# Performance work log

Hardware: AMD Instinct MI355X
Metric: run time of the kernel (lower is better)

The kernel has to match this reference:

```python
import jax, jax.numpy as jnp
import numpy as np
import math

N_HEAD = 16
ROPE_BASE = 10000.0


def _rope(xh):
    # xh: [B, H, T, D]; rotate full head dim using half-split (GPT-NeoX style)
    B, H, T, D = xh.shape
    theta = 1.0 / (ROPE_BASE ** (jnp.arange(0, D, 2, dtype=jnp.float32) / D))  # [D/2]
    idx_theta = jnp.arange(T, dtype=jnp.float32)[:, None] * theta[None, :]      # [T, D/2]
    idx_theta2 = jnp.concatenate([idx_theta, idx_theta], axis=1)                 # [T, D]
    cos = jnp.cos(idx_theta2)[None, None]                                        # [1,1,T,D]
    sin = jnp.sin(idx_theta2)[None, None]
    d2 = D // 2
    neg_half = jnp.concatenate([-xh[..., d2:], xh[..., :d2]], axis=-1)
    return xh * cos + neg_half * sin


def setup_inputs() -> dict:
    key = jax.random.key(0)
    k1, k2, k3 = jax.random.split(key, 3)
    B, T, C = 2, 2048, 2048
    x = jax.random.normal(k1, (B, T, C), dtype=jnp.float32)
    w_attn = jax.random.normal(k2, (C, 3 * C), dtype=jnp.float32) * (1.0 / math.sqrt(C))
    w_proj = jax.random.normal(k3, (C, C), dtype=jnp.float32) * (1.0 / math.sqrt(C))
    return {"x": x, "w_attn": w_attn, "w_proj": w_proj}


def reference(x, w_attn, w_proj):
    B, T, C = x.shape
    H = N_HEAD
    D = C // H
    qkv = x @ w_attn                                   # [B,T,3C]
    q, k, v = jnp.split(qkv, 3, axis=-1)
    # [B,T,C] -> [B,H,T,D]
    to_heads = lambda t: t.reshape(B, T, H, D).transpose(0, 2, 1, 3)
    q, k, v = to_heads(q), to_heads(k), to_heads(v)
    q = _rope(q)
    k = _rope(k)
    att = jnp.einsum('bhqd,bhkd->bhqk', q, k) * (1.0 / math.sqrt(D))
    causal = jnp.tril(jnp.ones((T, T), dtype=bool))
    att = jnp.where(causal[None, None], att, -jnp.inf)
    att = jax.nn.softmax(att, axis=-1)
    y = jnp.einsum('bhqk,bhkd->bhqd', att, v)          # [B,H,T,D]
    y = y.transpose(0, 2, 1, 3).reshape(B, T, C)
    return y @ w_proj
```

## Files before the change

kernel.cpp:

```cpp
#include <hip/hip_runtime.h>
#include <hip/hip_bf16.h>
#include <math.h>

typedef __bf16 bf16;
typedef __bf16 bf16x8 __attribute__((ext_vector_type(8)));
typedef float f32x4 __attribute__((ext_vector_type(4)));
typedef float f32x16 __attribute__((ext_vector_type(16)));
typedef unsigned int u32x2 __attribute__((ext_vector_type(2)));
typedef unsigned int u32x4 __attribute__((ext_vector_type(4)));

#define MFMA16(a, b, c) __builtin_amdgcn_mfma_f32_16x16x32_bf16((a), (b), (c), 0, 0, 0)
#define MFMA32(a, b, c) __builtin_amdgcn_mfma_f32_32x32x16_bf16((a), (b), (c), 0, 0, 0)

static constexpr int Bsz = 2, Tsz = 2048, Csz = 2048, Hn = 16, Dh = 128;
static constexpr float ATTN_SCALE = 0.08838834764831845f;

__device__ __forceinline__ void gld16(const void* src, void* dst) {
    __builtin_amdgcn_global_load_lds((__attribute__((address_space(1))) void*)src,
                                     (__attribute__((address_space(3))) void*)dst,
                                     16, 0, 0);
}

__device__ __forceinline__ unsigned cvt_pk_bf16(float lo, float hi) {
    unsigned r;
    asm("v_cvt_pk_bf16_f32 %0, %1, %2" : "=v"(r) : "v"(lo), "v"(hi));
    return r;
}

__device__ __forceinline__ bf16x8 make_pfrag(float p0, float p1, float p2, float p3,
                                             float p4, float p5, float p6, float p7) {
    unsigned a0 = cvt_pk_bf16(p0, p1), a1 = cvt_pk_bf16(p2, p3);
    unsigned b0 = cvt_pk_bf16(p4, p5), b1 = cvt_pk_bf16(p6, p7);
    asm volatile("v_permlane32_swap_b32 %0, %1" : "+v"(a0), "+v"(b0));
    asm volatile("v_permlane32_swap_b32 %0, %1" : "+v"(a1), "+v"(b1));
    u32x4 w = {a0, a1, b0, b1};
    return __builtin_bit_cast(bf16x8, w);
}

__global__ __launch_bounds__(256) void cast_x_kernel(const float* __restrict__ x,
                                                     bf16* __restrict__ o, int n8) {
    int i = blockIdx.x * 256 + threadIdx.x;
    if (i >= n8) return;
    const float4* x4 = (const float4*)x;
    float4 a = x4[2 * i], b = x4[2 * i + 1];
    bf16x8 v;
    v[0] = (bf16)a.x; v[1] = (bf16)a.y; v[2] = (bf16)a.z; v[3] = (bf16)a.w;
    v[4] = (bf16)b.x; v[5] = (bf16)b.y; v[6] = (bf16)b.z; v[7] = (bf16)b.w;
    ((bf16x8*)o)[i] = v;
}

template <typename TIN>
__global__ __launch_bounds__(256) void transpose_cast_kernel(const TIN* __restrict__ in,
                                                             bf16* __restrict__ out,
                                                             int R, int Cc) {
    __shared__ float tile[64][65];
    const int tx = threadIdx.x, ty = threadIdx.y;
    in  += (size_t)blockIdx.z * R * Cc;
    out += (size_t)blockIdx.z * R * Cc;
    const int c0 = blockIdx.x * 64, r0 = blockIdx.y * 64;
#pragma unroll
    for (int j = 0; j < 16; ++j) {
        int rr = ty + j * 4;
        tile[rr][tx] = (float)in[(size_t)(r0 + rr) * Cc + c0 + tx];
    }
    __syncthreads();
#pragma unroll
    for (int j = 0; j < 16; ++j) {
        int cc = ty + j * 4;
        out[(size_t)(c0 + cc) * R + r0 + tx] = (bf16)tile[tx][cc];
    }
}

__global__ __launch_bounds__(256) void cossin_kernel(float2* __restrict__ cs) {
    int idx = blockIdx.x * 256 + threadIdx.x;
    int t = idx >> 6, i = idx & 63;
    float theta = 1.0f / powf(10000.0f, (float)(2 * i) / 128.0f);
    float ang = (float)t * theta;
    cs[idx] = make_float2(cosf(ang), sinf(ang));
}

__global__ __launch_bounds__(512, 2)
void gemm384_qkv(const bf16* __restrict__ A, const bf16* __restrict__ Bt,
                 bf16* __restrict__ Oq, bf16* __restrict__ Ok, bf16* __restrict__ Ov,
                 const float2* __restrict__ cs, int K) {
    __shared__ bf16 sA[2][128 * 64];
    __shared__ bf16 sB[2][384 * 64];
    const int tid = threadIdx.x, lane = tid & 63, wid = tid >> 6;
    const int wm = wid >> 2, wn = wid & 3;
    const int lo16 = lane & 15, hi4 = lane >> 4;

    const int cpx = gridDim.x >> 3;
    const int swz = (blockIdx.x & 7) * cpx + (blockIdx.x >> 3);
    const int by = swz & 31;
    const int bx = swz >> 5;
    const int row0 = by << 7, col0 = bx * 384;

    const int srow = tid >> 3;
    const int swzoff = (((tid & 7) ^ ((tid >> 3) & 7)) << 3);
    const bf16* srcA = A  + (size_t)(row0 + srow) * K + swzoff;
    const bf16* srcB = Bt + (size_t)(col0 + srow) * K + swzoff;
    const size_t K64 = (size_t)K * 64;
    char* const ldsA = (char*)&sA[0][0];
    char* const ldsB = (char*)&sB[0][0];
    const int wuo = wid << 10;

    auto issueA = [&](int c, int kt) {
        const bf16* s = srcA + (size_t)kt * 64;
        gld16(s,       ldsA + c * 16384 + 0    + wuo);
        gld16(s + K64, ldsA + c * 16384 + 8192 + wuo);
    };
    auto issueB3lo = [&](int c, int kt) {
        const bf16* s = srcB + (size_t)kt * 64;
        gld16(s,           ldsB + c * 49152 + 0     + wuo);
        gld16(s + K64,     ldsB + c * 49152 + 8192  + wuo);
        gld16(s + 2 * K64, ldsB + c * 49152 + 16384 + wuo);
    };
    auto issueB3hi = [&](int c, int kt) {
        const bf16* s = srcB + (size_t)kt * 64 + 3 * K64;
        gld16(s,           ldsB + c * 49152 + 24576 + wuo);
        gld16(s + K64,     ldsB + c * 49152 + 32768 + wuo);
        gld16(s + 2 * K64, ldsB + c * 49152 + 40960 + wuo);
    };
    auto ldF = [&](const char* buf, int row, int ks) {
        return *(const bf16x8*)(buf + row * 128 + ((((ks << 2) + hi4) ^ (row & 7)) << 4));
    };

    const int arow = (wm << 6) + lo16;
    const int brow = (wn << 4) + lo16;

    f32x4 acc[4][6] = {};
    const int nkt = K >> 6;

    issueB3lo(0, 0); issueB3hi(0, 0); issueA(0, 0);
    if (nkt > 1) {
        issueA(1, 1);
        asm volatile("s_waitcnt vmcnt(2)" ::: "memory");
    } else {
        asm volatile("s_waitcnt vmcnt(0)" ::: "memory");
    }
    __builtin_amdgcn_s_barrier();

    for (int kt = 0; kt < nkt; ++kt) {
        const int c = kt & 1;
        const char* bufA = ldsA + c * 16384;
        const char* bufB = ldsB + c * 49152;
        bf16x8 af[4][2], bq[2][2];
#pragma unroll
        for (int i = 0; i < 4; ++i) {
            af[i][0] = ldF(bufA, arow + (i << 4), 0);
            af[i][1] = ldF(bufA, arow + (i << 4), 1);
        }
#pragma unroll
        for (int j = 0; j < 2; ++j) {
            bq[j][0] = ldF(bufB, brow + (j << 6), 0);
            bq[j][1] = ldF(bufB, brow + (j << 6), 1);
        }
        if (kt + 1 < nkt) issueB3lo(c ^ 1, kt + 1);
        __builtin_amdgcn_s_barrier();
        asm volatile("s_waitcnt lgkmcnt(0)" ::: "memory");
        __builtin_amdgcn_sched_barrier(0);
        __builtin_amdgcn_s_setprio(1);
#pragma unroll
        for (int ks = 0; ks < 2; ++ks)
#pragma unroll
            for (int i = 0; i < 4; ++i)
#pragma unroll
                for (int j = 0; j < 2; ++j)
                    acc[i][j] = MFMA16(af[i][ks], bq[j][ks], acc[i][j]);
        __builtin_amdgcn_s_setprio(0);
        __builtin_amdgcn_s_barrier();
#pragma unroll
        for (int j = 0; j < 2; ++j) {
            bq[j][0] = ldF(bufB, brow + ((j + 2) << 6), 0);
            bq[j][1] = ldF(bufB, brow + ((j + 2) << 6), 1);
        }
        if (kt + 1 < nkt) issueB3hi(c ^ 1, kt + 1);
        __builtin_amdgcn_s_barrier();
        asm volatile("s_waitcnt lgkmcnt(0)" ::: "memory");
        __builtin_amdgcn_sched_barrier(0);
        __builtin_amdgcn_s_setprio(1);
#pragma unroll
        for (int ks = 0; ks < 2; ++ks)
#pragma unroll
            for (int i = 0; i < 4; ++i)
#pragma unroll
                for (int j = 0; j < 2; ++j)
                    acc[i][j + 2] = MFMA16(af[i][ks], bq[j][ks], acc[i][j + 2]);
        __builtin_amdgcn_s_setprio(0);
        __builtin_amdgcn_s_barrier();
#pragma unroll
        for (int j = 0; j < 2; ++j) {
            bq[j][0] = ldF(bufB, brow + ((j + 4) << 6), 0);
            bq[j][1] = ldF(bufB, brow + ((j + 4) << 6), 1);
        }
        if (kt + 2 < nkt) issueA(c, kt + 2);
        __builtin_amdgcn_s_barrier();
        asm volatile("s_waitcnt lgkmcnt(0)" ::: "memory");
        __builtin_amdgcn_sched_barrier(0);
        __builtin_amdgcn_s_setprio(1);
#pragma unroll
        for (int ks = 0; ks < 2; ++ks)
#pragma unroll
            for (int i = 0; i < 4; ++i)
#pragma unroll
                for (int j = 0; j < 2; ++j)
                    acc[i][j + 4] = MFMA16(af[i][ks], bq[j][ks], acc[i][j + 4]);
        __builtin_amdgcn_s_setprio(0);
        if (kt + 2 < nkt)      asm volatile("s_waitcnt vmcnt(2)" ::: "memory");
        else if (kt + 1 < nkt) asm volatile("s_waitcnt vmcnt(0)" ::: "memory");
        __builtin_amdgcn_s_barrier();
    }

    const int d = (wn << 4) + lo16;
#pragma unroll
    for (int p = 0; p < 3; ++p) {
        const int gcb = col0 + (p << 7);
        const int seg = gcb >> 11;
        const int hb = (gcb >> 7) & 15;
        if (seg < 2) {
            bf16* dst0 = (seg == 0) ? Oq : Ok;
            const float qs = (seg == 0) ? ATTN_SCALE : 1.0f;
#pragma unroll
            for (int mi = 0; mi < 4; ++mi)
#pragma unroll
                for (int r = 0; r < 4; ++r) {
                    const int gm = row0 + (wm << 6) + (mi << 4) + (hi4 << 2) + r;
                    const int b = gm >> 11, t = gm & 2047;
                    const float2 csv = cs[t * 64 + d];
                    bf16* drow = dst0 + ((((size_t)b * Hn + hb) * Tsz + t) << 7);
                    const float vlo = acc[mi][2 * p][r];
                    const float vhi = acc[mi][2 * p + 1][r];
                    drow[d]      = (bf16)((vlo * csv.x - vhi * csv.y) * qs);
                    drow[d + 64] = (bf16)((vhi * csv.x + vlo * csv.y) * qs);
                }
        } else {
#pragma unroll
            for (int mi = 0; mi < 4; ++mi)
#pragma unroll
                for (int r = 0; r < 4; ++r) {
                    const int gm = row0 + (wm << 6) + (mi << 4) + (hi4 << 2) + r;
                    const int b = gm >> 11, t = gm & 2047;
                    bf16* drow = Ov + ((((size_t)b * Hn + hb) * Tsz + t) << 7);
                    drow[d]      = (bf16)acc[mi][2 * p][r];
                    drow[d + 64] = (bf16)acc[mi][2 * p + 1][r];
                }
        }
    }
}

__global__ __launch_bounds__(256)
void gemm128_bt(const bf16* __restrict__ A, const bf16* __restrict__ Bt,
                float* __restrict__ Cf, int M, int N, int K) {
    __shared__ bf16 sA[128 * 64];
    __shared__ bf16 sB[128 * 64];
    const int tid = threadIdx.x;
    const int lane = tid & 63, wv = tid >> 6;
    const int wr = wv >> 1, wc = wv & 1;
    const int lo16 = lane & 15, hi4 = lane >> 4;
    const int row0 = blockIdx.y << 7, col0 = blockIdx.x << 7;

    f32x4 acc[4][4] = {};

    const int nkt = K >> 6;
    for (int kt = 0; kt < nkt; ++kt) {
        const int kbase = kt << 6;
#pragma unroll
        for (int c = 0; c < 4; ++c) {
            const int o16 = (c << 8) + tid;
            const int row = o16 >> 3, u = o16 & 7;
            const int colel = kbase + ((u ^ (row & 7)) << 3);
            gld16(A  + (size_t)(row0 + row) * K + colel,
                  (char*)sA + (((c << 8) + (wv << 6)) << 4));
            gld16(Bt + (size_t)(col0 + row) * K + colel,
                  (char*)sB + (((c << 8) + (wv << 6)) << 4));
        }
        __syncthreads();
#pragma unroll
        for (int ks = 0; ks < 2; ++ks) {
            bf16x8 af[4], bfv[4];
#pragma unroll
            for (int mi = 0; mi < 4; ++mi) {
                const int ar = (wr << 6) + (mi << 4) + lo16;
                af[mi] = *(const bf16x8*)((const char*)sA + ar * 128 +
                          (((ks << 6) + (hi4 << 4)) ^ ((ar & 7) << 4)));
            }
#pragma unroll
            for (int ni = 0; ni < 4; ++ni) {
                const int bc = (wc << 4) + (ni << 5) + lo16;
                bfv[ni] = *(const bf16x8*)((const char*)sB + bc * 128 +
                           (((ks << 6) + (hi4 << 4)) ^ ((bc & 7) << 4)));
            }
#pragma unroll
            for (int mi = 0; mi < 4; ++mi)
#pragma unroll
                for (int ni = 0; ni < 4; ++ni)
                    acc[mi][ni] = MFMA16(af[mi], bfv[ni], acc[mi][ni]);
        }
        __syncthreads();
    }

#pragma unroll
    for (int mi = 0; mi < 4; ++mi)
#pragma unroll
        for (int r = 0; r < 4; ++r) {
            const int gm = row0 + (wr << 6) + (mi << 4) + (hi4 << 2) + r;
            float* crow = Cf + (size_t)gm * N + col0 + (wc << 4) + lo16;
#pragma unroll
            for (int ni = 0; ni < 4; ++ni)
                crow[ni << 5] = acc[mi][ni][r];
        }
}

__device__ __forceinline__ void stage_tile(const bf16* __restrict__ Kb,
                                           const bf16* __restrict__ Vtb,
                                           bf16* sKc, bf16* sVc, int k0, int tid) {
#pragma unroll
    for (int c = 0; c < 4; ++c) {
        const int off = (c << 12) + (tid << 4);
        const int row = off >> 8, u = (off >> 4) & 15;
        gld16(Kb + (size_t)(k0 + row) * Dh + ((u ^ (row & 7)) << 3), (char*)sKc + off);
        const int dv = off >> 7, uv = (off >> 4) & 7;
        gld16(Vtb + (size_t)dv * Tsz + k0 + ((uv ^ (dv & 7)) << 3), (char*)sVc + off);
    }
}

__global__ __launch_bounds__(256, 2)
void attn_kernel(const bf16* __restrict__ Q, const bf16* __restrict__ K,
                 const bf16* __restrict__ Vt, bf16* __restrict__ Y) {
    __shared__ bf16 sK[2][64 * 128];
    __shared__ bf16 sV[2][128 * 64];
    const int tid = threadIdx.x, lane = tid & 63, wv = tid >> 6;
    const int lo32 = lane & 31, hl = lane >> 5;

    const int i = blockIdx.x;
    const int g = i >> 5;
    const int bh = i & 31;
    const int t = (i < 256) ? (15 - g) : (g - 8);
    const int b = bh >> 4, h = bh & 15;

    const int q0 = t << 7;
    const int q0w = q0 + (wv << 5);
    const int qg = q0w + lo32;

    const bf16* Kb  = K  + (size_t)bh * (Tsz * Dh);
    const bf16* Vtb = Vt + (size_t)bh * (Tsz * Dh);
    const bf16* Qp  = Q  + (size_t)bh * (Tsz * Dh) + (size_t)qg * Dh;

    bf16x8 qf[8];
#pragma unroll
    for (int kc = 0; kc < 8; ++kc)
        qf[kc] = *(const bf16x8*)(Qp + (kc << 4) + (hl << 3));

    float m = -1e30f, lsum = 0.f;
    f32x16 o[4] = {};

    const int nt_block = 2 * t + 2;
    const int nt_warp = ((q0w + 31) >> 6) + 1;

    stage_tile(Kb, Vtb, &sK[0][0], &sV[0][0], 0, tid);

    int cur = 0;
    for (int kt = 0; kt < nt_block; ++kt) {
        __syncthreads();
        if (kt + 1 < nt_block)
            stage_tile(Kb, Vtb, &sK[cur ^ 1][0], &sV[cur ^ 1][0], (kt + 1) << 6, tid);
        if (kt < nt_warp) {
            const int k0 = kt << 6;
            const bf16* kbuf = &sK[cur][0];
            const bf16* vbuf = &sV[cur][0];
            f32x16 s0 = {}, s1 = {};
            const int swk = lo32 & 7;
            __builtin_amdgcn_s_setprio(1);
#pragma unroll
            for (int kc = 0; kc < 8; ++kc) {
                bf16x8 kf0 = *(const bf16x8*)((const char*)kbuf + lo32 * 256 +
                              ((((kc << 1) + hl) ^ swk) << 4));
                s0 = MFMA32(kf0, qf[kc], s0);
                bf16x8 kf1 = *(const bf16x8*)((const char*)kbuf + (32 + lo32) * 256 +
                              ((((kc << 1) + hl) ^ swk) << 4));
                s1 = MFMA32(kf1, qf[kc], s1);
            }
            __builtin_amdgcn_s_setprio(0);

            const bool bnd = (k0 + 63 > q0w);
            if (bnd) {
#pragma unroll
                for (int r = 0; r < 16; ++r) {
                    const int kl = (r & 3) + ((r >> 2) << 3) + (hl << 2);
                    if (k0 + kl > qg)      s0[r] = -1e30f;
                    if (k0 + 32 + kl > qg) s1[r] = -1e30f;
                }
            }
            float pm = s0[0];
#pragma unroll
            for (int r = 1; r < 16; ++r) pm = fmaxf(pm, s0[r]);
#pragma unroll
            for (int r = 0; r < 16; ++r) pm = fmaxf(pm, s1[r]);
            pm = fmaxf(pm, __shfl_xor(pm, 32));

            if (__any(pm > m + 8.0f)) {
                const float mn = fmaxf(m, pm);
                const float sc = __expf(m - mn);
                m = mn;
                lsum *= sc;
#pragma unroll
                for (int db = 0; db < 4; ++db)
#pragma unroll
                    for (int r = 0; r < 16; ++r) o[db][r] *= sc;
            }
            float rs = 0.f;
            if (bnd) {
#pragma unroll
                for (int r = 0; r < 16; ++r) {
                    float e0 = (s0[r] > -1e29f) ? __expf(s0[r] - m) : 0.f;
                    float e1 = (s1[r] > -1e29f) ? __expf(s1[r] - m) : 0.f;
                    s0[r] = e0; s1[r] = e1; rs += e0 + e1;
                }
            } else {
#pragma unroll
                for (int r = 0; r < 16; ++r) {
                    float e0 = __expf(s0[r] - m);
                    float e1 = __expf(s1[r] - m);
                    s0[r] = e0; s1[r] = e1; rs += e0 + e1;
                }
            }
            rs += __shfl_xor(rs, 32);
            lsum += rs;

            bf16x8 pb0 = make_pfrag(s0[0], s0[1], s0[2],  s0[3],  s0[4],  s0[5],  s0[6],  s0[7]);
            bf16x8 pb1 = make_pfrag(s0[8], s0[9], s0[10], s0[11], s0[12], s0[13], s0[14], s0[15]);
            bf16x8 pb2 = make_pfrag(s1[0], s1[1], s1[2],  s1[3],  s1[4],  s1[5],  s1[6],  s1[7]);
            bf16x8 pb3 = make_pfrag(s1[8], s1[9], s1[10], s1[11], s1[12], s1[13], s1[14], s1[15]);

            __builtin_amdgcn_s_setprio(1);
#pragma unroll
            for (int db = 0; db < 4; ++db) {
                const int rd = (db << 5) + lo32;
                const char* vrow = (const char*)vbuf + rd * 128;
                const int sw = rd & 7;
                bf16x8 v0 = *(const bf16x8*)(vrow + (((0 + hl) ^ sw) << 4));
                o[db] = MFMA32(v0, pb0, o[db]);
                bf16x8 v1 = *(const bf16x8*)(vrow + (((2 + hl) ^ sw) << 4));
                o[db] = MFMA32(v1, pb1, o[db]);
                bf16x8 v2 = *(const bf16x8*)(vrow + (((4 + hl) ^ sw) << 4));
                o[db] = MFMA32(v2, pb2, o[db]);
                bf16x8 v3 = *(const bf16x8*)(vrow + (((6 + hl) ^ sw) << 4));
                o[db] = MFMA32(v3, pb3, o[db]);
            }
            __builtin_amdgcn_s_setprio(0);
        }
        cur ^= 1;
    }

    const float inv = 1.0f / lsum;
    const size_t rowoff = ((size_t)b * Tsz + qg) * (size_t)Csz + (size_t)h * 128;
#pragma unroll
    for (int db = 0; db < 4; ++db)
#pragma unroll
        for (int gg = 0; gg < 4; ++gg) {
            unsigned w0 = cvt_pk_bf16(o[db][4 * gg + 0] * inv, o[db][4 * gg + 1] * inv);
            unsigned w1 = cvt_pk_bf16(o[db][4 * gg + 2] * inv, o[db][4 * gg + 3] * inv);
            u32x2 w = {w0, w1};
            *(u32x2*)(Y + rowoff + (db << 5) + (gg << 3) + (hl << 2)) = w;
        }
}

extern "C" void kernel_launch(void* const* d_in, const int* in_sizes, int n_in,
                              void* d_out, int out_size, void* d_ws, size_t ws_size,
                              hipStream_t stream) {
    const float* x      = (const float*)d_in[0];
    const float* w_attn = (const float*)d_in[1];
    const float* w_proj = (const float*)d_in[2];
    float* out = (float*)d_out;

    char* ws = (char*)d_ws;
    bf16* Xb  = (bf16*)(ws);
    bf16* Wat = (bf16*)(ws + 16777216);
    bf16* Wpt = (bf16*)(ws + 41943040);
    bf16* Qr  = (bf16*)(ws + 50331648);
    bf16* Kr  = (bf16*)(ws + 67108864);
    bf16* Vb  = (bf16*)(ws + 83886080);
    bf16* Vt  = (bf16*)(ws + 100663296);
    bf16* Yb  = (bf16*)(ws + 117440512);
    float2* cs = (float2*)(ws + 134217728);

    cast_x_kernel<<<4096, 256, 0, stream>>>(x, Xb, (Bsz * Tsz * Csz) / 8);
    transpose_cast_kernel<float><<<dim3(96, 32, 1), dim3(64, 4), 0, stream>>>(w_attn, Wat, 2048, 6144);
    transpose_cast_kernel<float><<<dim3(32, 32, 1), dim3(64, 4), 0, stream>>>(w_proj, Wpt, 2048, 2048);
    cossin_kernel<<<512, 256, 0, stream>>>(cs);

    gemm384_qkv<<<512, 512, 0, stream>>>(Xb, Wat, Qr, Kr, Vb, cs, 2048);
    transpose_cast_kernel<bf16><<<dim3(2, 32, 32), dim3(64, 4), 0, stream>>>(Vb, Vt, 2048, 128);

    attn_kernel<<<dim3(512), 256, 0, stream>>>(Qr, Kr, Vt, Yb);

    gemm128_bt<<<dim3(16, 32), 256, 0, stream>>>(Yb, Wpt, out, 4096, 2048, 2048);
}
```

Baseline: 243.8 us.

## Restructure QKV GEMM prefetch into progressive per-stage waits with peeled last iteration

Reorganizes the double-buffered global-to-LDS loading in the QKV projection GEMM. The next tile's A and B loads are now issued at the start of each iteration, and each sub-stage waits only for the B chunk it needs through graduated vmcnt waits. The final k-iteration is peeled so the steady-state loop carries no conditionals. The aim is to let later B chunks keep loading while MFMAs run on earlier chunks, shortening exposed load latency, at the cost of more code and tighter vmcnt bookkeeping that must stay correct.

```diff
diff --git a/kernel.cpp b/kernel.cpp
--- a/kernel.cpp
+++ b/kernel.cpp
@@ -109,17 +109,10 @@
         gld16(s,       ldsA + c * 16384 + 0    + wuo);
         gld16(s + K64, ldsA + c * 16384 + 8192 + wuo);
     };
-    auto issueB3lo = [&](int c, int kt) {
-        const bf16* s = srcB + (size_t)kt * 64;
-        gld16(s,           ldsB + c * 49152 + 0     + wuo);
-        gld16(s + K64,     ldsB + c * 49152 + 8192  + wuo);
-        gld16(s + 2 * K64, ldsB + c * 49152 + 16384 + wuo);
-    };
-    auto issueB3hi = [&](int c, int kt) {
-        const bf16* s = srcB + (size_t)kt * 64 + 3 * K64;
-        gld16(s,           ldsB + c * 49152 + 24576 + wuo);
-        gld16(s + K64,     ldsB + c * 49152 + 32768 + wuo);
-        gld16(s + 2 * K64, ldsB + c * 49152 + 40960 + wuo);
+    auto issueB = [&](int c, int kt, int u) {
+        const bf16* s = srcB + (size_t)kt * 64 + (size_t)(2 * u) * K64;
+        gld16(s,       ldsB + c * 49152 + u * 16384 + 0    + wuo);
+        gld16(s + K64, ldsB + c * 49152 + u * 16384 + 8192 + wuo);
     };
     auto ldF = [&](const char* buf, int row, int ks) {
         return *(const bf16x8*)(buf + row * 128 + ((((ks << 2) + hi4) ^ (row & 7)) << 4));
@@ -131,16 +124,11 @@
     f32x4 acc[4][6] = {};
     const int nkt = K >> 6;
 
-    issueB3lo(0, 0); issueB3hi(0, 0); issueA(0, 0);
-    if (nkt > 1) {
-        issueA(1, 1);
-        asm volatile("s_waitcnt vmcnt(2)" ::: "memory");
-    } else {
-        asm volatile("s_waitcnt vmcnt(0)" ::: "memory");
-    }
+    issueA(0, 0); issueB(0, 0, 0); issueB(0, 0, 1); issueB(0, 0, 2);
+    asm volatile("s_waitcnt vmcnt(4)" ::: "memory");
     __builtin_amdgcn_s_barrier();
 
-    for (int kt = 0; kt < nkt; ++kt) {
+    for (int kt = 0; kt < nkt - 1; ++kt) {
         const int c = kt & 1;
         const char* bufA = ldsA + c * 16384;
         const char* bufB = ldsB + c * 49152;
@@ -155,7 +143,7 @@
             bq[j][0] = ldF(bufB, brow + (j << 6), 0);
             bq[j][1] = ldF(bufB, brow + (j << 6), 1);
         }
-        if (kt + 1 < nkt) issueB3lo(c ^ 1, kt + 1);
+        issueA(c ^ 1, kt + 1); issueB(c ^ 1, kt + 1, 0); issueB(c ^ 1, kt + 1, 1);
         __builtin_amdgcn_s_barrier();
         asm volatile("s_waitcnt lgkmcnt(0)" ::: "memory");
         __builtin_amdgcn_sched_barrier(0);
@@ -168,13 +156,14 @@
                 for (int j = 0; j < 2; ++j)
                     acc[i][j] = MFMA16(af[i][ks], bq[j][ks], acc[i][j]);
         __builtin_amdgcn_s_setprio(0);
+        asm volatile("s_waitcnt vmcnt(8)" ::: "memory");
         __builtin_amdgcn_s_barrier();
 #pragma unroll
         for (int j = 0; j < 2; ++j) {
             bq[j][0] = ldF(bufB, brow + ((j + 2) << 6), 0);
             bq[j][1] = ldF(bufB, brow + ((j + 2) << 6), 1);
         }
-        if (kt + 1 < nkt) issueB3hi(c ^ 1, kt + 1);
+        issueB(c ^ 1, kt + 1, 2);
         __builtin_amdgcn_s_barrier();
         asm volatile("s_waitcnt lgkmcnt(0)" ::: "memory");
         __builtin_amdgcn_sched_barrier(0);
@@ -187,13 +176,13 @@
                 for (int j = 0; j < 2; ++j)
                     acc[i][j + 2] = MFMA16(af[i][ks], bq[j][ks], acc[i][j + 2]);
         __builtin_amdgcn_s_setprio(0);
+        asm volatile("s_waitcnt vmcnt(8)" ::: "memory");
         __builtin_amdgcn_s_barrier();
 #pragma unroll
         for (int j = 0; j < 2; ++j) {
             bq[j][0] = ldF(bufB, brow + ((j + 4) << 6), 0);
             bq[j][1] = ldF(bufB, brow + ((j + 4) << 6), 1);
         }
-        if (kt + 2 < nkt) issueA(c, kt + 2);
         __builtin_amdgcn_s_barrier();
         asm volatile("s_waitcnt lgkmcnt(0)" ::: "memory");
         __builtin_amdgcn_sched_barrier(0);
@@ -206,9 +195,75 @@
                 for (int j = 0; j < 2; ++j)
                     acc[i][j + 4] = MFMA16(af[i][ks], bq[j][ks], acc[i][j + 4]);
         __builtin_amdgcn_s_setprio(0);
-        if (kt + 2 < nkt)      asm volatile("s_waitcnt vmcnt(2)" ::: "memory");
-        else if (kt + 1 < nkt) asm volatile("s_waitcnt vmcnt(0)" ::: "memory");
-        __builtin_amdgcn_s_barrier();
+        asm volatile("s_waitcnt vmcnt(4)" ::: "memory");
+        __builtin_amdgcn_s_barrier();
+    }
+
+    {
+        const int c = (nkt - 1) & 1;
+        const char* bufA = ldsA + c * 16384;
+        const char* bufB = ldsB + c * 49152;
+        bf16x8 af[4][2], bq[2][2];
+#pragma unroll
+        for (int i = 0; i < 4; ++i) {
+            af[i][0] = ldF(bufA, arow + (i << 4), 0);
+            af[i][1] = ldF(bufA, arow + (i << 4), 1);
+        }
+#pragma unroll
+        for (int j = 0; j < 2; ++j) {
+            bq[j][0] = ldF(bufB, brow + (j << 6), 0);
+            bq[j][1] = ldF(bufB, brow + (j << 6), 1);
+        }
+        __builtin_amdgcn_s_barrier();
+        asm volatile("s_waitcnt lgkmcnt(0)" ::: "memory");
+        __builtin_amdgcn_sched_barrier(0);
+        __builtin_amdgcn_s_setprio(1);
+#pragma unroll
+        for (int ks = 0; ks < 2; ++ks)
+#pragma unroll
+            for (int i = 0; i < 4; ++i)
+#pragma unroll
+                for (int j = 0; j < 2; ++j)
+                    acc[i][j] = MFMA16(af[i][ks], bq[j][ks], acc[i][j]);
+        __builtin_amdgcn_s_setprio(0);
+        asm volatile("s_waitcnt vmcnt(2)" ::: "memory");
+        __builtin_amdgcn_s_barrier();
+#pragma unroll
+        for (int j = 0; j < 2; ++j) {
+            bq[j][0] = ldF(bufB, brow + ((j + 2) << 6), 0);
+            bq[j][1] = ldF(bufB, brow + ((j + 2) << 6), 1);
+        }
+        __builtin_amdgcn_s_barrier();
+        asm volatile("s_waitcnt lgkmcnt(0)" ::: "memory");
+        __builtin_amdgcn_sched_barrier(0);
+        __builtin_amdgcn_s_setprio(1);
+#pragma unroll
+        for (int ks = 0; ks < 2; ++ks)
+#pragma unroll
+            for (int i = 0; i < 4; ++i)
+#pragma unroll
+                for (int j = 0; j < 2; ++j)
+                    acc[i][j + 2] = MFMA16(af[i][ks], bq[j][ks], acc[i][j + 2]);
+        __builtin_amdgcn_s_setprio(0);
+        asm volatile("s_waitcnt vmcnt(0)" ::: "memory");
+        __builtin_amdgcn_s_barrier();
+#pragma unroll
+        for (int j = 0; j < 2; ++j) {
+            bq[j][0] = ldF(bufB, brow + ((j + 4) << 6), 0);
+            bq[j][1] = ldF(bufB, brow + ((j + 4) << 6), 1);
+        }
+        __builtin_amdgcn_s_barrier();
+        asm volatile("s_waitcnt lgkmcnt(0)" ::: "memory");
+        __builtin_amdgcn_sched_barrier(0);
+        __builtin_amdgcn_s_setprio(1);
+#pragma unroll
+        for (int ks = 0; ks < 2; ++ks)
+#pragma unroll
+            for (int i = 0; i < 4; ++i)
+#pragma unroll
+                for (int j = 0; j < 2; ++j)
+                    acc[i][j + 4] = MFMA16(af[i][ks], bq[j][ks], acc[i][j + 4]);
+        __builtin_amdgcn_s_setprio(0);
     }
 
     const int d = (wn << 4) + lo16;
```

Result: no change. 241.5 us (-0.9%).

## Restructure QKV GEMM main loop into four quadrant phases with finer B prefetch

Applied to the files above, without the earlier changes.

The QKV projection GEMM's K-loop is reorganised from three phases (all A fragments times two B column groups each) into four quadrant phases (half of the A rows times half of the B columns). B tile loads are split into three two-row-group chunks, issued at different phases, with one chunk prefetched two iterations ahead. The intent is to cut register pressure for the A fragments, reuse B fragments across two phases, and spread global-to-LDS traffic more evenly to overlap it with MFMA work. It adds an extra barrier pair and relies on more delicate vmcnt bookkeeping that must match the issue order exactly.

```diff
diff --git a/kernel.cpp b/kernel.cpp
--- a/kernel.cpp
+++ b/kernel.cpp
@@ -109,17 +109,10 @@
         gld16(s,       ldsA + c * 16384 + 0    + wuo);
         gld16(s + K64, ldsA + c * 16384 + 8192 + wuo);
     };
-    auto issueB3lo = [&](int c, int kt) {
-        const bf16* s = srcB + (size_t)kt * 64;
-        gld16(s,           ldsB + c * 49152 + 0     + wuo);
-        gld16(s + K64,     ldsB + c * 49152 + 8192  + wuo);
-        gld16(s + 2 * K64, ldsB + c * 49152 + 16384 + wuo);
-    };
-    auto issueB3hi = [&](int c, int kt) {
-        const bf16* s = srcB + (size_t)kt * 64 + 3 * K64;
-        gld16(s,           ldsB + c * 49152 + 24576 + wuo);
-        gld16(s + K64,     ldsB + c * 49152 + 32768 + wuo);
-        gld16(s + 2 * K64, ldsB + c * 49152 + 40960 + wuo);
+    auto issueB = [&](int c, int kt, int u) {
+        const bf16* s = srcB + (size_t)kt * 64 + (size_t)(2 * u) * K64;
+        gld16(s,       ldsB + c * 49152 + u * 16384 + 0    + wuo);
+        gld16(s + K64, ldsB + c * 49152 + u * 16384 + 8192 + wuo);
     };
     auto ldF = [&](const char* buf, int row, int ks) {
         return *(const bf16x8*)(buf + row * 128 + ((((ks << 2) + hi4) ^ (row & 7)) << 4));
@@ -131,31 +124,27 @@
     f32x4 acc[4][6] = {};
     const int nkt = K >> 6;
 
-    issueB3lo(0, 0); issueB3hi(0, 0); issueA(0, 0);
-    if (nkt > 1) {
-        issueA(1, 1);
-        asm volatile("s_waitcnt vmcnt(2)" ::: "memory");
-    } else {
-        asm volatile("s_waitcnt vmcnt(0)" ::: "memory");
-    }
+    issueA(0, 0); issueB(0, 0, 0); issueB(0, 0, 1); issueB(0, 0, 2);
+    if (nkt > 1) { issueA(1, 1); issueB(1, 1, 0); }
+    asm volatile("s_waitcnt vmcnt(6)" ::: "memory");
     __builtin_amdgcn_s_barrier();
 
     for (int kt = 0; kt < nkt; ++kt) {
         const int c = kt & 1;
         const char* bufA = ldsA + c * 16384;
         const char* bufB = ldsB + c * 49152;
-        bf16x8 af[4][2], bq[2][2];
-#pragma unroll
-        for (int i = 0; i < 4; ++i) {
-            af[i][0] = ldF(bufA, arow + (i << 4), 0);
-            af[i][1] = ldF(bufA, arow + (i << 4), 1);
-        }
-#pragma unroll
-        for (int j = 0; j < 2; ++j) {
+        bf16x8 a0[2][2], a1[2][2], bq[3][2];
+#pragma unroll
+        for (int mi = 0; mi < 2; ++mi) {
+            a0[mi][0] = ldF(bufA, arow + (mi << 4), 0);
+            a0[mi][1] = ldF(bufA, arow + (mi << 4), 1);
+        }
+#pragma unroll
+        for (int j = 0; j < 3; ++j) {
             bq[j][0] = ldF(bufB, brow + (j << 6), 0);
             bq[j][1] = ldF(bufB, brow + (j << 6), 1);
         }
-        if (kt + 1 < nkt) issueB3lo(c ^ 1, kt + 1);
+        if (kt + 1 < nkt) issueB(c ^ 1, kt + 1, 1);
         __builtin_amdgcn_s_barrier();
         asm volatile("s_waitcnt lgkmcnt(0)" ::: "memory");
         __builtin_amdgcn_sched_barrier(0);
@@ -163,18 +152,18 @@
 #pragma unroll
         for (int ks = 0; ks < 2; ++ks)
 #pragma unroll
-            for (int i = 0; i < 4; ++i)
-#pragma unroll
-                for (int j = 0; j < 2; ++j)
-                    acc[i][j] = MFMA16(af[i][ks], bq[j][ks], acc[i][j]);
+            for (int mi = 0; mi < 2; ++mi)
+#pragma unroll
+                for (int j = 0; j < 3; ++j)
+                    acc[mi][j] = MFMA16(a0[mi][ks], bq[j][ks], acc[mi][j]);
         __builtin_amdgcn_s_setprio(0);
         __builtin_amdgcn_s_barrier();
 #pragma unroll
-        for (int j = 0; j < 2; ++j) {
-            bq[j][0] = ldF(bufB, brow + ((j + 2) << 6), 0);
-            bq[j][1] = ldF(bufB, brow + ((j + 2) << 6), 1);
-        }
-        if (kt + 1 < nkt) issueB3hi(c ^ 1, kt + 1);
+        for (int mi = 0; mi < 2; ++mi) {
+            a1[mi][0] = ldF(bufA, arow + 32 + (mi << 4), 0);
+            a1[mi][1] = ldF(bufA, arow + 32 + (mi << 4), 1);
+        }
+        if (kt + 1 < nkt) issueB(c ^ 1, kt + 1, 2);
         __builtin_amdgcn_s_barrier();
         asm volatile("s_waitcnt lgkmcnt(0)" ::: "memory");
         __builtin_amdgcn_sched_barrier(0);
@@ -182,16 +171,18 @@
 #pragma unroll
         for (int ks = 0; ks < 2; ++ks)
 #pragma unroll
-            for (int i = 0; i < 4; ++i)
-#pragma unroll
-                for (int j = 0; j < 2; ++j)
-                    acc[i][j + 2] = MFMA16(af[i][ks], bq[j][ks], acc[i][j + 2]);
+            for (int mi = 0; mi < 2; ++mi)
+#pragma unroll
+                for (int j = 0; j < 3; ++j)
+                    acc[mi + 2][j] = MFMA16(a1[mi][ks], bq[j][ks], acc[mi + 2][j]);
         __builtin_amdgcn_s_setprio(0);
-        __builtin_amdgcn_s_barrier();
-#pragma unroll
-        for (int j = 0; j < 2; ++j) {
-            bq[j][0] = ldF(bufB, brow + ((j + 4) << 6), 0);
-            bq[j][1] = ldF(bufB, brow + ((j + 4) << 6), 1);
+        if (kt + 1 < nkt) asm volatile("s_waitcnt vmcnt(8)" ::: "memory");
+        else              asm volatile("s_waitcnt vmcnt(0)" ::: "memory");
+        __builtin_amdgcn_s_barrier();
+#pragma unroll
+        for (int j = 0; j < 3; ++j) {
+            bq[j][0] = ldF(bufB, brow + 192 + (j << 6), 0);
+            bq[j][1] = ldF(bufB, brow + 192 + (j << 6), 1);
         }
         if (kt + 2 < nkt) issueA(c, kt + 2);
         __builtin_amdgcn_s_barrier();
@@ -201,13 +192,25 @@
 #pragma unroll
         for (int ks = 0; ks < 2; ++ks)
 #pragma unroll
-            for (int i = 0; i < 4; ++i)
-#pragma unroll
-                for (int j = 0; j < 2; ++j)
-                    acc[i][j + 4] = MFMA16(af[i][ks], bq[j][ks], acc[i][j + 4]);
+            for (int mi = 0; mi < 2; ++mi)
+#pragma unroll
+                for (int j = 0; j < 3; ++j)
+                    acc[mi + 2][j + 3] = MFMA16(a1[mi][ks], bq[j][ks], acc[mi + 2][j + 3]);
         __builtin_amdgcn_s_setprio(0);
-        if (kt + 2 < nkt)      asm volatile("s_waitcnt vmcnt(2)" ::: "memory");
-        else if (kt + 1 < nkt) asm volatile("s_waitcnt vmcnt(0)" ::: "memory");
+        __builtin_amdgcn_s_barrier();
+        if (kt + 2 < nkt) issueB(c, kt + 2, 0);
+        __builtin_amdgcn_s_barrier();
+        __builtin_amdgcn_s_setprio(1);
+#pragma unroll
+        for (int ks = 0; ks < 2; ++ks)
+#pragma unroll
+            for (int mi = 0; mi < 2; ++mi)
+#pragma unroll
+                for (int j = 0; j < 3; ++j)
+                    acc[mi][j + 3] = MFMA16(a0[mi][ks], bq[j][ks], acc[mi][j + 3]);
+        __builtin_amdgcn_s_setprio(0);
+        if (kt + 2 < nkt)      asm volatile("s_waitcnt vmcnt(6)" ::: "memory");
+        else if (kt + 1 < nkt) asm volatile("s_waitcnt vmcnt(2)" ::: "memory");
         __builtin_amdgcn_s_barrier();
     }
 
```

Measured after the change: 260.4 us. 6.8% more time.
